# Performance work log

Measured on AMD Instinct MI355X. Metric: run time of the kernel, lower is better.

Reference implementation:

```python
import jax, jax.numpy as jnp
import numpy as np

# SMPL constants and module defaults
NV, NF, T, S = 6890, 13776, 3, 256
NEAR, FAR = 0.1, 25.0
VIEW_ANGLE = 30.0
EYE = np.array([0.0, 0.0, -(1.0 / np.tan(np.radians(VIEW_ANGLE)) + 1.0)], np.float32)
AMB_INT, DIR_INT = 1.0, 0.0
AMB_COL = np.array([1.0, 1.0, 1.0], np.float32)
DIR_COL = np.array([1.0, 1.0, 1.0], np.float32)
LIGHT_DIR = np.array([0.0, 1.0, 0.0], np.float32)
BG = np.array([0.0, 0.0, 0.0], np.float32)
CHUNK = 128  # faces processed per z-buffer scan step


def _coords(t):
    # create_coords: (2, T*T) barycentric-style grid over [0,1]^2 (torch meshgrid 'ij')
    step = 1.0 / (t - 1) if t > 1 else 1.0
    ab = np.arange(0.0, 1.0 + step * 0.5, step, dtype=np.float32)
    xv, yv = np.meshgrid(ab, ab, indexing='ij')
    return jnp.asarray(np.stack([xv.ravel(), yv.ravel()], 0))

COORDS = _coords(T)


def _grid_sample(img, grid):
    # F.grid_sample: bilinear, zeros padding, align_corners=False
    # img (B,C,H,W), grid (B,N,M,2) in [-1,1] -> (B,C,N,M)
    Bc, C, H, W = img.shape
    gx = (grid[..., 0] + 1.0) * (W * 0.5) - 0.5
    gy = (grid[..., 1] + 1.0) * (H * 0.5) - 0.5
    x0 = jnp.floor(gx)
    y0 = jnp.floor(gy)
    fx = gx - x0
    fy = gy - y0

    def tap(xi, yi, w):
        valid = (xi >= 0) & (xi < W) & (yi >= 0) & (yi < H)
        xc = jnp.clip(xi, 0, W - 1).astype(jnp.int32)
        yc = jnp.clip(yi, 0, H - 1).astype(jnp.int32)
        v = jax.vmap(lambda im, y, x: im[:, y, x])(img, yc, xc)  # (B,C,N,M)
        return v * (w * valid)[:, None]

    return (tap(x0, y0, (1 - fx) * (1 - fy)) + tap(x0 + 1, y0, fx * (1 - fy))
            + tap(x0, y0 + 1, (1 - fx) * fy) + tap(x0 + 1, y0 + 1, fx * fy))


def _rasterize_one(f3, tex):
    # f3: (NF,3,3) camera-space face vertices (x,y in [-1,1] screen, z depth)
    # tex: (NF,T,T,T,3) per-face texture cube. Z-buffer rasterization (NMR-style,
    # CCW front faces only, perspective-correct depth and texture weights).
    F = f3.shape[0]
    pad = (-F) % CHUNK
    f3p = jnp.concatenate([f3, jnp.zeros((pad, 3, 3), f3.dtype)], 0)
    nc = f3p.shape[0] // CHUNK
    chunks = f3p.reshape(nc, CHUNK, 3, 3)
    bases = jnp.arange(nc, dtype=jnp.int32) * CHUNK
    yi, xi = jnp.meshgrid(jnp.arange(S), jnp.arange(S), indexing='ij')
    px = ((2.0 * xi.ravel() + 1.0 - S) / S).astype(f3.dtype)  # (P,)
    py = ((2.0 * yi.ravel() + 1.0 - S) / S).astype(f3.dtype)
    P = S * S

    @jax.checkpoint
    def step(carry, inp):
        zbuf, fid, wbuf = carry
        base, fc = inp
        vx = fc[:, :, 0][..., None]  # (C,3,1)
        vy = fc[:, :, 1][..., None]
        vz = fc[:, :, 2]             # (C,3)
        x0, x1, x2 = vx[:, 0], vx[:, 1], vx[:, 2]
        y0, y1, y2 = vy[:, 0], vy[:, 1], vy[:, 2]
        det = (x1 - x0) * (y2 - y0) - (y1 - y0) * (x2 - x0)  # (C,1)
        e0 = (x1 - px) * (y2 - py) - (y1 - py) * (x2 - px)   # (C,P)
        e1 = (x2 - px) * (y0 - py) - (y2 - py) * (x0 - px)
        e2 = (x0 - px) * (y1 - py) - (y0 - py) * (x1 - px)
        den = jnp.where(jnp.abs(det) > 1e-10, det, 1.0)
        b0, b1, b2 = e0 / den, e1 / den, e2 / den
        zs = jnp.where(jnp.abs(vz) > 1e-8, vz, 1.0)  # (C,3)
        inv_z = b0 / zs[:, 0:1] + b1 / zs[:, 1:2] + b2 / zs[:, 2:3]
        inv_z = jnp.where(jnp.abs(inv_z) > 1e-8, inv_z, 1.0)
        zp = 1.0 / inv_z  # perspective-correct depth at pixel
        inside = (det > 1e-10) & (e0 >= 0) & (e1 >= 0) & (e2 >= 0)
        valid = inside & (zp > NEAR) & (zp < FAR)
        zm = jnp.where(valid, zp, jnp.inf)
        best = jnp.argmin(zm, axis=0)  # (P,)
        bz = jnp.take_along_axis(zm, best[None], 0)[0]
        w = jnp.stack([jnp.take_along_axis(b0, best[None], 0)[0],
                       jnp.take_along_axis(b1, best[None], 0)[0],
                       jnp.take_along_axis(b2, best[None], 0)[0]], -1)  # (P,3)
        zv = zs[best]  # (P,3)
        bzf = jnp.where(jnp.isfinite(bz), bz, 0.0)
        wpc = (w / zv) * bzf[:, None]  # perspective-correct barycentric
        upd = bz < zbuf
        zbuf = jnp.where(upd, bz, zbuf)
        fid = jnp.where(upd, base + best.astype(jnp.int32), fid)
        wbuf = jnp.where(upd[:, None], wpc, wbuf)
        return (zbuf, fid, wbuf), None

    init = (jnp.full((P,), jnp.inf, f3.dtype),
            jnp.full((P,), -1, jnp.int32),
            jnp.zeros((P, 3), f3.dtype))
    (zbuf, fid, wbuf), _ = jax.lax.scan(step, init, (bases, chunks))

    # trilinear texture-cube sampling at barycentric position
    fg = fid >= 0
    fidc = jnp.clip(fid, 0, F - 1)
    pos = jnp.clip(wbuf, 0.0, 1.0) * (T - 1)  # (P,3)
    i0 = jnp.clip(jnp.floor(pos), 0, max(T - 2, 0)).astype(jnp.int32)
    fr = jnp.clip(pos - i0, 0.0, 1.0)
    col = jnp.zeros((P, 3), f3.dtype)
    for d0 in (0, 1):
        for d1 in (0, 1):
            for d2 in (0, 1):
                wgt = ((fr[:, 0] if d0 else 1 - fr[:, 0])
                       * (fr[:, 1] if d1 else 1 - fr[:, 1])
                       * (fr[:, 2] if d2 else 1 - fr[:, 2]))
                c = tex[fidc,
                        jnp.minimum(i0[:, 0] + d0, T - 1),
                        jnp.minimum(i0[:, 1] + d1, T - 1),
                        jnp.minimum(i0[:, 2] + d2, T - 1)]  # (P,3)
                col = col + wgt[:, None] * c
    img = jnp.where(fg[:, None], col, jnp.asarray(BG, f3.dtype))
    return img.reshape(S, S, 3).transpose(2, 0, 1)  # (3,S,S)


def _forward(cam, vertices, uv_imgs, faces):
    B = cam.shape[0]
    # --- dynamic_sampler: orthographic projection + per-face barycentric UV grid ---
    pts2d = cam[:, None, 0:1] * (vertices[:, :, :2] + cam[:, None, 1:3])  # (B,NV,2)
    f2pts = pts2d[:, faces]                                               # (B,NF,3,2)
    v2 = f2pts[:, :, 2]
    mat = jnp.stack([f2pts[:, :, 0] - v2, f2pts[:, :, 1] - v2], axis=-1)  # (B,NF,2,2)
    sampler = jnp.einsum('bfik,kt->bfti', mat, COORDS) + v2[:, :, None, :]
    sampler = jnp.clip(sampler, -1.0, 1.0)                                # (B,NF,T*T,2)
    # --- extract_tex ---
    tex = _grid_sample(uv_imgs, sampler)                                  # (B,3,NF,T*T)
    tex = tex.reshape(B, 3, NF, T, T).transpose(0, 2, 3, 4, 1)            # (B,NF,T,T,3)
    textures = jnp.repeat(tex[:, :, :, :, None, :], T, axis=4)            # (B,NF,T,T,T,3)
    # --- lighting (defaults: ambient=1, directional=0 -> identity; kept general) ---
    fverts = vertices[:, faces]  # (B,NF,3,3)
    n = jnp.cross(fverts[:, :, 1] - fverts[:, :, 0], fverts[:, :, 2] - fverts[:, :, 0])
    n = n / (jnp.linalg.norm(n, axis=-1, keepdims=True) + 1e-10)
    ldir = jnp.asarray(LIGHT_DIR / np.linalg.norm(LIGHT_DIR))
    cos = jax.nn.relu(n @ ldir)
    light = AMB_INT * jnp.asarray(AMB_COL) + DIR_INT * jnp.asarray(DIR_COL) * cos[..., None]
    tex_lit = textures * light[:, :, None, None, None, :]
    # --- projection (y flipped) + look_at ---
    proj = jnp.concatenate([pts2d[..., 0:1], -pts2d[..., 1:2], vertices[:, :, 2:3]], -1)
    eye = jnp.asarray(EYE)
    z_ax = -eye / jnp.linalg.norm(eye)
    x_ax = jnp.cross(jnp.array([0.0, 1.0, 0.0], proj.dtype), z_ax)
    x_ax = x_ax / jnp.linalg.norm(x_ax)
    y_ax = jnp.cross(z_ax, x_ax)
    R = jnp.stack([x_ax, y_ax, z_ax])  # (3,3)
    vcam = (proj - eye) @ R.T
    f3 = vcam[:, faces]  # (B,NF,3,3)
    images = jax.vmap(_rasterize_one)(f3, tex_lit)  # (B,3,S,S)
    return images, textures


def setup_inputs() -> dict:
    key = jax.random.key(0)
    k1, k2, k3, k4 = jax.random.split(key, 4)
    cam = jax.random.uniform(k1, (1, 3), dtype=jnp.float32)
    vertices = jax.random.normal(k2, (1, NV, 3), dtype=jnp.float32)
    uv_imgs = jax.random.uniform(k3, (1, 3, 256, 256), dtype=jnp.float32)
    faces = jax.random.randint(k4, (NF, 3), 0, NV, dtype=jnp.int32)
    return {"cam": cam, "vertices": vertices, "uv_imgs": uv_imgs, "faces": faces}


def reference(cam, vertices, uv_imgs, faces):
    return _forward(cam, vertices, uv_imgs, faces)
```

## Files before the change

### kernel.cpp

```cpp
#include <hip/hip_runtime.h>

#define NVERT 6890
#define NFACE 13776
#define SS 256
#define NPIX (SS*SS)
#define TILE 8
#define NSB 256
#define SPLIT 16
#define SEGLEN 861
#define SENTINEL 0x7F800000FFFFFFFFULL
#define ZBASE 0x3D000000u

#define OFF_KEYS 0u
#define OFF_VB   524288u
#define OFF_FD   607232u
#define OFF_HIST 1488896u
#define OFF_CURS 1489920u
#define OFF_TD2  1490944u

static __device__ __forceinline__ unsigned int zbucket(unsigned int zmb) {
  return (zmb > ZBASE) ? min(255u, (zmb - ZBASE) >> 19) : 0u;
}

static __device__ __forceinline__ float edgef(float ax, float ay, float bx, float by,
                                              float px, float py) {
  return __fsub_rn(__fmul_rn(__fsub_rn(ax, px), __fsub_rn(by, py)),
                   __fmul_rn(__fsub_rn(ay, py), __fsub_rn(bx, px)));
}

__global__ __launch_bounds__(256) void prep_k(const float* __restrict__ cam,
                                              const float* __restrict__ verts,
                                              float* __restrict__ vb,
                                              unsigned long long* __restrict__ keys,
                                              unsigned int* __restrict__ hist) {
  int i = blockIdx.x * 256 + threadIdx.x;
  keys[i] = SENTINEL;
  if (i < 256) hist[i] = 0u;
  if (i < NVERT) {
    float c0 = cam[0], c1 = cam[1], c2 = cam[2];
    float vx = verts[i*3+0], vy = verts[i*3+1], vz = verts[i*3+2];
    vb[i*3+0] = __fmul_rn(c0, __fadd_rn(vx, c1));
    vb[i*3+1] = __fmul_rn(c0, __fadd_rn(vy, c2));
    vb[i*3+2] = __fadd_rn(vz, 2.7320508075688776f);
  }
}

__global__ __launch_bounds__(256) void tex_k(const float* __restrict__ vb,
                                             const int* __restrict__ faces,
                                             const float* __restrict__ uv,
                                             float* __restrict__ out_tex) {
  int tid = blockIdx.x * 256 + threadIdx.x;
  if (tid >= NFACE * 9) return;
  int f = tid / 9, t = tid - f * 9;
  int ti = t / 3, tj = t - ti * 3;
  float xt = 0.5f * (float)ti;
  float yt = 0.5f * (float)tj;
  int ia = faces[f*3+0], ib = faces[f*3+1], ic = faces[f*3+2];
  float ax = vb[ia*3+0], ay = vb[ia*3+1];
  float bx = vb[ib*3+0], by = vb[ib*3+1];
  float cx = vb[ic*3+0], cy = vb[ic*3+1];
  float sx = (ax - cx) * xt + (bx - cx) * yt + cx;
  float sy = (ay - cy) * xt + (by - cy) * yt + cy;
  sx = fminf(fmaxf(sx, -1.f), 1.f);
  sy = fminf(fmaxf(sy, -1.f), 1.f);
  float gx = (sx + 1.f) * 128.f - 0.5f;
  float gy = (sy + 1.f) * 128.f - 0.5f;
  float x0f = floorf(gx), y0f = floorf(gy);
  float fx = gx - x0f, fy = gy - y0f;
  int x0 = (int)x0f, y0 = (int)y0f;
  float r = 0.f, g = 0.f, b = 0.f;
  #pragma unroll
  for (int dy = 0; dy < 2; ++dy) {
    #pragma unroll
    for (int dx = 0; dx < 2; ++dx) {
      int xi = x0 + dx, yi = y0 + dy;
      if (xi >= 0 && xi < SS && yi >= 0 && yi < SS) {
        float w = (dx ? fx : 1.f - fx) * (dy ? fy : 1.f - fy);
        int base = yi * SS + xi;
        r += w * uv[base];
        g += w * uv[NPIX + base];
        b += w * uv[2 * NPIX + base];
      }
    }
  }
  float* ot = out_tex + f * 81 + ti * 27 + tj * 9;
  #pragma unroll
  for (int kk = 0; kk < 3; ++kk) {
    ot[kk*3+0] = r; ot[kk*3+1] = g; ot[kk*3+2] = b;
  }
}

__global__ __launch_bounds__(256) void setup_k(const float* __restrict__ vb,
                                               const int* __restrict__ faces,
                                               float* __restrict__ fd,
                                               unsigned int* __restrict__ hist) {
  int f = blockIdx.x * 256 + threadIdx.x;
  if (f >= NFACE) return;
  float* fp = fd + (size_t)f * 16;
  int ia = faces[f*3+0], ib = faces[f*3+1], ic = faces[f*3+2];
  float x0 = vb[ia*3+0], y0 = -vb[ia*3+1], z0 = vb[ia*3+2];
  float x1 = vb[ib*3+0], y1 = -vb[ib*3+1], z1 = vb[ib*3+2];
  float x2 = vb[ic*3+0], y2 = -vb[ic*3+1], z2 = vb[ic*3+2];
  float det = edgef(x1, y1, x2, y2, x0, y0);
  unsigned int tilepack = 0x000000FFu;
  if (det > 1e-10f) {
    float mnx = fminf(x0, fminf(x1, x2)), mxx = fmaxf(x0, fmaxf(x1, x2));
    float mny = fminf(y0, fminf(y1, y2)), mxy = fmaxf(y0, fmaxf(y1, y2));
    int xlo = max((int)floorf((mnx * 256.f + 255.f) * 0.5f) - 2, 0);
    int xhi = min((int)ceilf ((mxx * 256.f + 255.f) * 0.5f) + 2, SS - 1);
    int ylo = max((int)floorf((mny * 256.f + 255.f) * 0.5f) - 2, 0);
    int yhi = min((int)ceilf ((mxy * 256.f + 255.f) * 0.5f) + 2, SS - 1);
    if (xlo <= xhi && ylo <= yhi)
      tilepack = (unsigned int)(xlo >> 3) | ((unsigned int)(ylo >> 3) << 8)
               | ((unsigned int)(xhi >> 3) << 16) | ((unsigned int)(yhi >> 3) << 24);
  }
  float rz0 = (fabsf(z0) > 1e-8f) ? z0 : 1.0f;
  float rz1 = (fabsf(z1) > 1e-8f) ? z1 : 1.0f;
  float rz2 = (fabsf(z2) > 1e-8f) ? z2 : 1.0f;
  float minrz = fminf(fminf(fabsf(rz0), fabsf(rz1)), fabsf(rz2));
  unsigned int flag = (minrz < 0.05f) ? 1u : 0u;
  unsigned int zmb = 0u;
  if (flag == 0u) {
    float mn = fminf(fminf(rz0, rz1), rz2);
    if (mn > 0.f) zmb = __float_as_uint(mn * 0.999f);
  }
  fp[0] = x0;  fp[1] = y0;  fp[2] = x1;  fp[3] = y1;
  fp[4] = x2;  fp[5] = y2;  fp[6] = rz0; fp[7] = rz1;
  fp[8] = rz2; fp[9] = det;
  fp[10] = __fdiv_rn(1.0f, det * rz0);
  fp[11] = __fdiv_rn(1.0f, det * rz1);
  fp[12] = __fdiv_rn(1.0f, det * rz2);
  fp[13] = __uint_as_float((unsigned int)f | (flag << 24));
  fp[14] = __uint_as_float(tilepack);
  fp[15] = __uint_as_float(zmb);
  atomicAdd(&hist[zbucket(zmb)], 1u);
}

__global__ __launch_bounds__(256) void bscan_k(const unsigned int* __restrict__ hist,
                                               unsigned int* __restrict__ curs) {
  __shared__ unsigned int bsh[256];
  int tid = threadIdx.x;
  unsigned int v = hist[tid];
  bsh[tid] = v;
  __syncthreads();
  for (int off = 1; off < 256; off <<= 1) {
    unsigned int t = (tid >= off) ? bsh[tid - off] : 0u;
    __syncthreads();
    bsh[tid] += t;
    __syncthreads();
  }
  curs[tid] = bsh[tid] - v;
}

__global__ __launch_bounds__(256) void scatter_k(const float* __restrict__ fd,
                                                 unsigned int* __restrict__ curs,
                                                 uint4* __restrict__ td2) {
  int f = blockIdx.x * 256 + threadIdx.x;
  if (f >= NFACE) return;
  const float* fp = fd + (size_t)f * 16;
  unsigned int tilepack = __float_as_uint(fp[14]);
  unsigned int zmb      = __float_as_uint(fp[15]);
  unsigned int slot = atomicAdd(&curs[zbucket(zmb)], 1u);
  unsigned int pos = (slot & 15u) * SEGLEN + (slot >> 4);
  td2[pos] = make_uint4(tilepack, zmb, (unsigned int)f, 0u);
}

__global__ __launch_bounds__(256) void tile_k(const float* __restrict__ fd,
                                              const uint4* __restrict__ td2,
                                              unsigned long long* __restrict__ keys) {
  __shared__ unsigned short idx_s[4][256];
  __shared__ unsigned int cnt_s[4];
  __shared__ unsigned int wmax_s[4];
  int sb  = blockIdx.x & (NSB - 1);
  int seg = blockIdx.x >> 8;
  int tid = threadIdx.x;
  int w = tid >> 6, lane = tid & 63;
  int sbx = sb & 15, sby = sb >> 4;
  int tx = sbx * 2 + (w & 1);
  int ty = sby * 2 + (w >> 1);
  int xx = tx * TILE + (lane & 7);
  int yy = ty * TILE + (lane >> 3);
  float px = (float)(2 * xx + 1 - SS) * (1.0f / 256.0f);
  float py = (float)(2 * yy + 1 - SS) * (1.0f / 256.0f);
  int p = yy * SS + xx;
  unsigned long long best = SENTINEL;
  unsigned long long lastw = SENTINEL;
  const uint4* tseg = td2 + (size_t)seg * SEGLEN;

  for (int base = 0; base < SEGLEN; base += 256) {
    unsigned int gz = (unsigned int)(keys[p] >> 32);
    unsigned int kz = min((unsigned int)(best >> 32), gz);
    unsigned int bh = kz;
    #pragma unroll
    for (int o = 32; o > 0; o >>= 1)
      bh = max(bh, (unsigned int)__shfl_xor((int)bh, o, 64));
    __syncthreads();
    if (lane == 0) wmax_s[w] = bh;
    if (tid < 4) cnt_s[tid] = 0;
    __syncthreads();
    unsigned int bm = max(max(wmax_s[0], wmax_s[1]), max(wmax_s[2], wmax_s[3]));
    unsigned int z0 = tseg[base].y;
    unsigned int b0 = zbucket(z0);
    unsigned int lb = b0 ? (ZBASE + (b0 << 19)) : 0u;
    if (lb > bm) break;
    int fi = base + tid;
    if (fi < SEGLEN) {
      uint4 t2 = tseg[fi];
      unsigned int tp = t2.x, zmb = t2.y;
      int tx0 = (int)(tp & 255u),         ty0 = (int)((tp >> 8) & 255u);
      int tx1 = (int)((tp >> 16) & 255u), ty1 = (int)(tp >> 24);
      #pragma unroll
      for (int q = 0; q < 4; ++q) {
        int qtx = sbx * 2 + (q & 1);
        int qty = sby * 2 + (q >> 1);
        if (qtx >= tx0 && qtx <= tx1 && qty >= ty0 && qty <= ty1
            && zmb <= wmax_s[q]) {
          unsigned int slot = atomicAdd(&cnt_s[q], 1u);
          idx_s[q][slot] = (unsigned short)t2.z;
        }
      }
    }
    __syncthreads();
    int m = (int)cnt_s[w];
    for (int j = 0; j < m; ++j) {
      int f2 = __builtin_amdgcn_readfirstlane((int)idx_s[w][j]);
      const float4* fr = (const float4*)(fd + (size_t)f2 * 16);
      float4 A  = fr[0];
      float4 Bv = fr[1];
      float4 Cv = fr[2];
      float4 Dv = fr[3];
      unsigned int zmb = __float_as_uint(Dv.w);
      if (zmb > kz) continue;
      float e0 = edgef(A.z, A.w, Bv.x, Bv.y, px, py);
      float e1 = edgef(Bv.x, Bv.y, A.x, A.y, px, py);
      float e2 = edgef(A.x, A.y, A.z, A.w, px, py);
      if (e0 >= 0.f && e1 >= 0.f && e2 >= 0.f) {
        float inva = __fmaf_rn(e0, Cv.z, __fmaf_rn(e1, Cv.w, e2 * Dv.x));
        float zc = __uint_as_float(kz);
        unsigned int w13 = __float_as_uint(Dv.y);
        bool pass = ((w13 >> 24) != 0u) | (inva * zc > 0.998f) | (fabsf(inva) < 1e-4f);
        if (pass) {
          float rz0 = Bv.z, rz1 = Bv.w, rz2 = Cv.x, det = Cv.y;
          float b0f = __fdiv_rn(e0, det);
          float b1f = __fdiv_rn(e1, det);
          float b2f = __fdiv_rn(e2, det);
          float inv = __fadd_rn(__fadd_rn(__fdiv_rn(b0f, rz0), __fdiv_rn(b1f, rz1)),
                                __fdiv_rn(b2f, rz2));
          if (!(fabsf(inv) > 1e-8f)) inv = 1.0f;
          float zp = __fdiv_rn(1.0f, inv);
          if (zp > 0.1f && zp < 25.0f) {
            unsigned long long key =
                ((unsigned long long)__float_as_uint(zp) << 32)
                | (w13 & 0x00FFFFFFu);
            if (key < best) {
              best = key;
              kz = min(kz, (unsigned int)(best >> 32));
            }
          }
        }
      }
    }
    if (best != lastw && (unsigned int)(best >> 32) <= gz) {
      atomicMin(&keys[p], best);
      lastw = best;
    }
  }
}

__global__ __launch_bounds__(256) void resolve_k(const float* __restrict__ vb,
                                                 const int* __restrict__ faces,
                                                 const unsigned long long* __restrict__ keys,
                                                 const float* __restrict__ out_tex,
                                                 float* __restrict__ out_img) {
  int p = blockIdx.x * 256 + threadIdx.x;
  if (p >= NPIX) return;
  unsigned long long k = keys[p];
  float c0 = 0.f, c1 = 0.f, c2 = 0.f;
  if (k != SENTINEL) {
    int f = (int)(unsigned int)(k & 0x00FFFFFFULL);
    float bz = __uint_as_float((unsigned int)(k >> 32));
    int xx = p & (SS - 1), yy = p >> 8;
    float px = (float)(2 * xx + 1 - SS) * (1.0f / 256.0f);
    float py = (float)(2 * yy + 1 - SS) * (1.0f / 256.0f);
    int ia = faces[f*3+0], ib = faces[f*3+1], ic = faces[f*3+2];
    float x0 = vb[ia*3+0], y0 = -vb[ia*3+1], z0 = vb[ia*3+2];
    float x1 = vb[ib*3+0], y1 = -vb[ib*3+1], z1 = vb[ib*3+2];
    float x2 = vb[ic*3+0], y2 = -vb[ic*3+1], z2 = vb[ic*3+2];
    float det = edgef(x1, y1, x2, y2, x0, y0);
    float e0 = edgef(x1, y1, x2, y2, px, py);
    float e1 = edgef(x2, y2, x0, y0, px, py);
    float e2 = edgef(x0, y0, x1, y1, px, py);
    float b0 = __fdiv_rn(e0, det);
    float b1 = __fdiv_rn(e1, det);
    float b2 = __fdiv_rn(e2, det);
    float rz0 = (fabsf(z0) > 1e-8f) ? z0 : 1.0f;
    float rz1 = (fabsf(z1) > 1e-8f) ? z1 : 1.0f;
    float rz2 = (fabsf(z2) > 1e-8f) ? z2 : 1.0f;
    float w0 = __fmul_rn(__fdiv_rn(b0, rz0), bz);
    float w1 = __fmul_rn(__fdiv_rn(b1, rz1), bz);
    float w2 = __fmul_rn(__fdiv_rn(b2, rz2), bz);
    float pos0 = fminf(fmaxf(w0, 0.f), 1.f) * 2.f;
    float pos1 = fminf(fmaxf(w1, 0.f), 1.f) * 2.f;
    float pos2 = fminf(fmaxf(w2, 0.f), 1.f) * 2.f;
    float i0f = fminf(fmaxf(floorf(pos0), 0.f), 1.f);
    float i1f = fminf(fmaxf(floorf(pos1), 0.f), 1.f);
    float i2f = fminf(fmaxf(floorf(pos2), 0.f), 1.f);
    float fr0 = fminf(fmaxf(__fsub_rn(pos0, i0f), 0.f), 1.f);
    float fr1 = fminf(fmaxf(__fsub_rn(pos1, i1f), 0.f), 1.f);
    float fr2 = fminf(fmaxf(__fsub_rn(pos2, i2f), 0.f), 1.f);
    int i00 = (int)i0f, i01 = (int)i1f;
    #pragma unroll
    for (int d0 = 0; d0 < 2; ++d0) {
      float wa = d0 ? fr0 : __fsub_rn(1.f, fr0);
      #pragma unroll
      for (int d1 = 0; d1 < 2; ++d1) {
        float wb = d1 ? fr1 : __fsub_rn(1.f, fr1);
        int a = min(i00 + d0, 2);
        int b = min(i01 + d1, 2);
        const float* tp = &out_tex[f * 81 + a * 27 + b * 9];
        float wab = __fmul_rn(wa, wb);
        #pragma unroll
        for (int d2 = 0; d2 < 2; ++d2) {
          float wc = d2 ? fr2 : __fsub_rn(1.f, fr2);
          float wgt = __fmul_rn(wab, wc);
          c0 = __fadd_rn(c0, __fmul_rn(wgt, tp[0]));
          c1 = __fadd_rn(c1, __fmul_rn(wgt, tp[1]));
          c2 = __fadd_rn(c2, __fmul_rn(wgt, tp[2]));
        }
      }
    }
  }
  out_img[p]          = c0;
  out_img[NPIX + p]   = c1;
  out_img[2*NPIX + p] = c2;
}

extern "C" void kernel_launch(void* const* d_in, const int* in_sizes, int n_in,
                              void* d_out, int out_size, void* d_ws, size_t ws_size,
                              hipStream_t stream) {
  const float* cam   = (const float*)d_in[0];
  const float* verts = (const float*)d_in[1];
  const float* uv    = (const float*)d_in[2];
  const int*   faces = (const int*)d_in[3];
  float* out_img = (float*)d_out;
  float* out_tex = (float*)d_out + 3 * NPIX;

  char* ws = (char*)d_ws;
  unsigned long long* keys = (unsigned long long*)(ws + OFF_KEYS);
  float* vb          = (float*)(ws + OFF_VB);
  float* fd          = (float*)(ws + OFF_FD);
  unsigned int* hist = (unsigned int*)(ws + OFF_HIST);
  unsigned int* curs = (unsigned int*)(ws + OFF_CURS);
  uint4* td2         = (uint4*)(ws + OFF_TD2);

  prep_k<<<NPIX / 256, 256, 0, stream>>>(cam, verts, vb, keys, hist);
  tex_k<<<(NFACE * 9 + 255) / 256, 256, 0, stream>>>(vb, faces, uv, out_tex);
  setup_k<<<(NFACE + 255) / 256, 256, 0, stream>>>(vb, faces, fd, hist);
  bscan_k<<<1, 256, 0, stream>>>(hist, curs);
  scatter_k<<<(NFACE + 255) / 256, 256, 0, stream>>>(fd, curs, td2);
  tile_k<<<NSB * SPLIT, 256, 0, stream>>>(fd, td2, keys);
  resolve_k<<<NPIX / 256, 256, 0, stream>>>(vb, faces, keys, out_tex, out_img);
}
```

Baseline: 190.9 us.

## Eliminate prep and scan kernels by inlining vertex transform and per-block scan

```diff
diff --git a/kernel.cpp b/kernel.cpp
--- a/kernel.cpp
+++ b/kernel.cpp
@@ -8,15 +8,15 @@
 #define NSB 256
 #define SPLIT 16
 #define SEGLEN 861
-#define SENTINEL 0x7F800000FFFFFFFFULL
+#define SENTINEL 0xFFFFFFFFFFFFFFFFULL
 #define ZBASE 0x3D000000u
+#define EYEZ 2.7320508075688776f
 
 #define OFF_KEYS 0u
-#define OFF_VB   524288u
-#define OFF_FD   607232u
-#define OFF_HIST 1488896u
-#define OFF_CURS 1489920u
-#define OFF_TD2  1490944u
+#define OFF_FD   524288u
+#define OFF_HIST 1405952u
+#define OFF_CURS 1406976u
+#define OFF_TD2  1408000u
 
 static __device__ __forceinline__ unsigned int zbucket(unsigned int zmb) {
   return (zmb > ZBASE) ? min(255u, (zmb - ZBASE) >> 19) : 0u;
@@ -28,24 +28,8 @@
                    __fmul_rn(__fsub_rn(ay, py), __fsub_rn(bx, px)));
 }
 
-__global__ __launch_bounds__(256) void prep_k(const float* __restrict__ cam,
-                                              const float* __restrict__ verts,
-                                              float* __restrict__ vb,
-                                              unsigned long long* __restrict__ keys,
-                                              unsigned int* __restrict__ hist) {
-  int i = blockIdx.x * 256 + threadIdx.x;
-  keys[i] = SENTINEL;
-  if (i < 256) hist[i] = 0u;
-  if (i < NVERT) {
-    float c0 = cam[0], c1 = cam[1], c2 = cam[2];
-    float vx = verts[i*3+0], vy = verts[i*3+1], vz = verts[i*3+2];
-    vb[i*3+0] = __fmul_rn(c0, __fadd_rn(vx, c1));
-    vb[i*3+1] = __fmul_rn(c0, __fadd_rn(vy, c2));
-    vb[i*3+2] = __fadd_rn(vz, 2.7320508075688776f);
-  }
-}
-
-__global__ __launch_bounds__(256) void tex_k(const float* __restrict__ vb,
+__global__ __launch_bounds__(256) void tex_k(const float* __restrict__ cam,
+                                             const float* __restrict__ verts,
                                              const int* __restrict__ faces,
                                              const float* __restrict__ uv,
                                              float* __restrict__ out_tex) {
@@ -55,10 +39,14 @@
   int ti = t / 3, tj = t - ti * 3;
   float xt = 0.5f * (float)ti;
   float yt = 0.5f * (float)tj;
+  float c0 = cam[0], c1 = cam[1], c2 = cam[2];
   int ia = faces[f*3+0], ib = faces[f*3+1], ic = faces[f*3+2];
-  float ax = vb[ia*3+0], ay = vb[ia*3+1];
-  float bx = vb[ib*3+0], by = vb[ib*3+1];
-  float cx = vb[ic*3+0], cy = vb[ic*3+1];
+  float ax = __fmul_rn(c0, __fadd_rn(verts[ia*3+0], c1));
+  float ay = __fmul_rn(c0, __fadd_rn(verts[ia*3+1], c2));
+  float bx = __fmul_rn(c0, __fadd_rn(verts[ib*3+0], c1));
+  float by = __fmul_rn(c0, __fadd_rn(verts[ib*3+1], c2));
+  float cx = __fmul_rn(c0, __fadd_rn(verts[ic*3+0], c1));
+  float cy = __fmul_rn(c0, __fadd_rn(verts[ic*3+1], c2));
   float sx = (ax - cx) * xt + (bx - cx) * yt + cx;
   float sy = (ay - cy) * xt + (by - cy) * yt + cy;
   sx = fminf(fmaxf(sx, -1.f), 1.f);
@@ -90,17 +78,25 @@
   }
 }
 
-__global__ __launch_bounds__(256) void setup_k(const float* __restrict__ vb,
+__global__ __launch_bounds__(256) void setup_k(const float* __restrict__ cam,
+                                               const float* __restrict__ verts,
                                                const int* __restrict__ faces,
                                                float* __restrict__ fd,
                                                unsigned int* __restrict__ hist) {
   int f = blockIdx.x * 256 + threadIdx.x;
   if (f >= NFACE) return;
   float* fp = fd + (size_t)f * 16;
+  float c0 = cam[0], c1 = cam[1], c2 = cam[2];
   int ia = faces[f*3+0], ib = faces[f*3+1], ic = faces[f*3+2];
-  float x0 = vb[ia*3+0], y0 = -vb[ia*3+1], z0 = vb[ia*3+2];
-  float x1 = vb[ib*3+0], y1 = -vb[ib*3+1], z1 = vb[ib*3+2];
-  float x2 = vb[ic*3+0], y2 = -vb[ic*3+1], z2 = vb[ic*3+2];
+  float x0 =  __fmul_rn(c0, __fadd_rn(verts[ia*3+0], c1));
+  float y0 = -__fmul_rn(c0, __fadd_rn(verts[ia*3+1], c2));
+  float z0 =  __fadd_rn(verts[ia*3+2], EYEZ);
+  float x1 =  __fmul_rn(c0, __fadd_rn(verts[ib*3+0], c1));
+  float y1 = -__fmul_rn(c0, __fadd_rn(verts[ib*3+1], c2));
+  float z1 =  __fadd_rn(verts[ib*3+2], EYEZ);
+  float x2 =  __fmul_rn(c0, __fadd_rn(verts[ic*3+0], c1));
+  float y2 = -__fmul_rn(c0, __fadd_rn(verts[ic*3+1], c2));
+  float z2 =  __fadd_rn(verts[ic*3+2], EYEZ);
   float det = edgef(x1, y1, x2, y2, x0, y0);
   unsigned int tilepack = 0x000000FFu;
   if (det > 1e-10f) {
@@ -136,8 +132,10 @@
   atomicAdd(&hist[zbucket(zmb)], 1u);
 }
 
-__global__ __launch_bounds__(256) void bscan_k(const unsigned int* __restrict__ hist,
-                                               unsigned int* __restrict__ curs) {
+__global__ __launch_bounds__(256) void scatter_k(const float* __restrict__ fd,
+                                                 const unsigned int* __restrict__ hist,
+                                                 unsigned int* __restrict__ curs,
+                                                 uint4* __restrict__ td2) {
   __shared__ unsigned int bsh[256];
   int tid = threadIdx.x;
   unsigned int v = hist[tid];
@@ -149,18 +147,13 @@
     bsh[tid] += t;
     __syncthreads();
   }
-  curs[tid] = bsh[tid] - v;
-}
-
-__global__ __launch_bounds__(256) void scatter_k(const float* __restrict__ fd,
-                                                 unsigned int* __restrict__ curs,
-                                                 uint4* __restrict__ td2) {
-  int f = blockIdx.x * 256 + threadIdx.x;
+  int f = blockIdx.x * 256 + tid;
   if (f >= NFACE) return;
   const float* fp = fd + (size_t)f * 16;
   unsigned int tilepack = __float_as_uint(fp[14]);
   unsigned int zmb      = __float_as_uint(fp[15]);
-  unsigned int slot = atomicAdd(&curs[zbucket(zmb)], 1u);
+  unsigned int b = zbucket(zmb);
+  unsigned int slot = (bsh[b] - hist[b]) + atomicAdd(&curs[b], 1u);
   unsigned int pos = (slot & 15u) * SEGLEN + (slot >> 4);
   td2[pos] = make_uint4(tilepack, zmb, (unsigned int)f, 0u);
 }
@@ -238,7 +231,8 @@
         float inva = __fmaf_rn(e0, Cv.z, __fmaf_rn(e1, Cv.w, e2 * Dv.x));
         float zc = __uint_as_float(kz);
         unsigned int w13 = __float_as_uint(Dv.y);
-        bool pass = ((w13 >> 24) != 0u) | (inva * zc > 0.998f) | (fabsf(inva) < 1e-4f);
+        bool pass = (kz >= 0x7F800000u)
+                  | ((w13 >> 24) != 0u) | (inva * zc > 0.998f) | (fabsf(inva) < 1e-4f);
         if (pass) {
           float rz0 = Bv.z, rz1 = Bv.w, rz2 = Cv.x, det = Cv.y;
           float b0f = __fdiv_rn(e0, det);
@@ -267,7 +261,8 @@
   }
 }
 
-__global__ __launch_bounds__(256) void resolve_k(const float* __restrict__ vb,
+__global__ __launch_bounds__(256) void resolve_k(const float* __restrict__ cam,
+                                                 const float* __restrict__ verts,
                                                  const int* __restrict__ faces,
                                                  const unsigned long long* __restrict__ keys,
                                                  const float* __restrict__ out_tex,
@@ -275,17 +270,24 @@
   int p = blockIdx.x * 256 + threadIdx.x;
   if (p >= NPIX) return;
   unsigned long long k = keys[p];
-  float c0 = 0.f, c1 = 0.f, c2 = 0.f;
+  float c0v = 0.f, c1v = 0.f, c2v = 0.f;
   if (k != SENTINEL) {
     int f = (int)(unsigned int)(k & 0x00FFFFFFULL);
     float bz = __uint_as_float((unsigned int)(k >> 32));
     int xx = p & (SS - 1), yy = p >> 8;
     float px = (float)(2 * xx + 1 - SS) * (1.0f / 256.0f);
     float py = (float)(2 * yy + 1 - SS) * (1.0f / 256.0f);
+    float c0 = cam[0], c1 = cam[1], c2 = cam[2];
     int ia = faces[f*3+0], ib = faces[f*3+1], ic = faces[f*3+2];
-    float x0 = vb[ia*3+0], y0 = -vb[ia*3+1], z0 = vb[ia*3+2];
-    float x1 = vb[ib*3+0], y1 = -vb[ib*3+1], z1 = vb[ib*3+2];
-    float x2 = vb[ic*3+0], y2 = -vb[ic*3+1], z2 = vb[ic*3+2];
+    float x0 =  __fmul_rn(c0, __fadd_rn(verts[ia*3+0], c1));
+    float y0 = -__fmul_rn(c0, __fadd_rn(verts[ia*3+1], c2));
+    float z0 =  __fadd_rn(verts[ia*3+2], EYEZ);
+    float x1 =  __fmul_rn(c0, __fadd_rn(verts[ib*3+0], c1));
+    float y1 = -__fmul_rn(c0, __fadd_rn(verts[ib*3+1], c2));
+    float z1 =  __fadd_rn(verts[ib*3+2], EYEZ);
+    float x2 =  __fmul_rn(c0, __fadd_rn(verts[ic*3+0], c1));
+    float y2 = -__fmul_rn(c0, __fadd_rn(verts[ic*3+1], c2));
+    float z2 =  __fadd_rn(verts[ic*3+2], EYEZ);
     float det = edgef(x1, y1, x2, y2, x0, y0);
     float e0 = edgef(x1, y1, x2, y2, px, py);
     float e1 = edgef(x2, y2, x0, y0, px, py);
@@ -323,16 +325,16 @@
         for (int d2 = 0; d2 < 2; ++d2) {
           float wc = d2 ? fr2 : __fsub_rn(1.f, fr2);
           float wgt = __fmul_rn(wab, wc);
-          c0 = __fadd_rn(c0, __fmul_rn(wgt, tp[0]));
-          c1 = __fadd_rn(c1, __fmul_rn(wgt, tp[1]));
-          c2 = __fadd_rn(c2, __fmul_rn(wgt, tp[2]));
+          c0v = __fadd_rn(c0v, __fmul_rn(wgt, tp[0]));
+          c1v = __fadd_rn(c1v, __fmul_rn(wgt, tp[1]));
+          c2v = __fadd_rn(c2v, __fmul_rn(wgt, tp[2]));
         }
       }
     }
   }
-  out_img[p]          = c0;
-  out_img[NPIX + p]   = c1;
-  out_img[2*NPIX + p] = c2;
+  out_img[p]          = c0v;
+  out_img[NPIX + p]   = c1v;
+  out_img[2*NPIX + p] = c2v;
 }
 
 extern "C" void kernel_launch(void* const* d_in, const int* in_sizes, int n_in,
@@ -347,17 +349,16 @@
 
   char* ws = (char*)d_ws;
   unsigned long long* keys = (unsigned long long*)(ws + OFF_KEYS);
-  float* vb          = (float*)(ws + OFF_VB);
   float* fd          = (float*)(ws + OFF_FD);
   unsigned int* hist = (unsigned int*)(ws + OFF_HIST);
   unsigned int* curs = (unsigned int*)(ws + OFF_CURS);
   uint4* td2         = (uint4*)(ws + OFF_TD2);
 
-  prep_k<<<NPIX / 256, 256, 0, stream>>>(cam, verts, vb, keys, hist);
-  tex_k<<<(NFACE * 9 + 255) / 256, 256, 0, stream>>>(vb, faces, uv, out_tex);
-  setup_k<<<(NFACE + 255) / 256, 256, 0, stream>>>(vb, faces, fd, hist);
-  bscan_k<<<1, 256, 0, stream>>>(hist, curs);
-  scatter_k<<<(NFACE + 255) / 256, 256, 0, stream>>>(fd, curs, td2);
+  hipMemsetAsync(keys, 0xFF, (size_t)NPIX * 8, stream);
+  hipMemsetAsync(hist, 0, 2048, stream);
+  setup_k<<<(NFACE + 255) / 256, 256, 0, stream>>>(cam, verts, faces, fd, hist);
+  tex_k<<<(NFACE * 9 + 255) / 256, 256, 0, stream>>>(cam, verts, faces, uv, out_tex);
+  scatter_k<<<(NFACE + 255) / 256, 256, 0, stream>>>(fd, hist, curs, td2);
   tile_k<<<NSB * SPLIT, 256, 0, stream>>>(fd, td2, keys);
-  resolve_k<<<NPIX / 256, 256, 0, stream>>>(vb, faces, keys, out_tex, out_img);
-}
+  resolve_k<<<NPIX / 256, 256, 0, stream>>>(cam, verts, faces, keys, out_tex, out_img);
+}
```

New measurement: 191.7 us. Within noise of the previous version (+0.4%).
